# Performance work log

Measured on AMD Instinct MI355X. Metric: run time of the kernel, lower is better.

## Reference

```python
import jax, jax.numpy as jnp
import numpy as np

N = 50000       # nodes
E = 1600000     # edges (avg degree 32)
DIN = 64
DOUT = 64
DE = 16
ATT_SLOPE = 0.2   # leaky_relu slope inside attention (GAT standard)
ACT_SLOPE = 0.01  # F.leaky_relu default between layers


def setup_inputs() -> dict:
    key = jax.random.key(0)
    ks = jax.random.split(key, 16)

    def lin(k, i, o):
        return jax.random.normal(k, (i, o), jnp.float32) / np.sqrt(i).astype(np.float32)

    def vec(k, d):
        return jax.random.normal(k, (d,), jnp.float32) / np.sqrt(d).astype(np.float32)

    return {
        "X": jax.random.normal(ks[0], (N, DIN), jnp.float32),
        "edge_index": jax.random.randint(ks[1], (2, E), 0, N),
        "edge_attr": jax.random.normal(ks[2], (E, DE), jnp.float32),
        # layer 1 params
        "W1": lin(ks[3], DIN, DOUT), "We1": lin(ks[4], DE, DOUT),
        "as1": vec(ks[5], DOUT), "ad1": vec(ks[6], DOUT), "ae1": vec(ks[7], DOUT),
        "b1": jnp.zeros((DOUT,), jnp.float32),
        # layer 2 params
        "W2": lin(ks[8], DOUT, DOUT), "We2": lin(ks[9], DE, DOUT),
        "as2": vec(ks[10], DOUT), "ad2": vec(ks[11], DOUT), "ae2": vec(ks[12], DOUT),
        "b2": jnp.zeros((DOUT,), jnp.float32),
    }


def _gat_conv(x, src, dst, edge_attr, W, We, a_s, a_d, a_e, b):
    """GATConv with edge features, softmax attention over dst neighborhoods, max aggregation."""
    n = x.shape[0]
    h = x @ W                      # [N, DOUT]
    e = edge_attr @ We             # [E, DOUT]
    # per-edge attention logits
    logits = jax.nn.leaky_relu((h @ a_s)[src] + (h @ a_d)[dst] + e @ a_e, ATT_SLOPE)  # [E]
    # numerically-stable segment softmax over destination node
    m = jax.ops.segment_max(logits, dst, num_segments=n)      # [N]
    p = jnp.exp(logits - m[dst])                               # [E]
    s = jax.ops.segment_sum(p, dst, num_segments=n)            # [N]
    att = p / jnp.maximum(s[dst], 1e-16)                       # [E]
    msg = (h[src] + e) * att[:, None]                          # [E, DOUT]
    out = jax.ops.segment_max(msg, dst, num_segments=n)        # [N, DOUT], -inf for empty
    out = jnp.where(jnp.isfinite(out), out, 0.0)
    return out + b


def reference(X, edge_index, edge_attr,
              W1, We1, as1, ad1, ae1, b1,
              W2, We2, as2, ad2, ae2, b2):
    src, dst = edge_index[0], edge_index[1]
    c1 = _gat_conv(X, src, dst, edge_attr, W1, We1, as1, ad1, ae1, b1)
    c1 = jax.nn.leaky_relu(c1, ACT_SLOPE)
    c2 = _gat_conv(c1, src, dst, edge_attr, W2, We2, as2, ad2, ae2, b2)
    c2 = jax.nn.leaky_relu(c2, ACT_SLOPE)
    return c2
```

## Files before the change

### kernel.cpp

```cpp
#include <hip/hip_runtime.h>
#include <cstdint>
#include <cstddef>

#define NN 50000
#define EE 1600000
#define D  64
#define DE 16

typedef __attribute__((ext_vector_type(2))) float vf2;

__device__ __forceinline__ float bf2f(unsigned short u) {
    return __uint_as_float(((unsigned)u) << 16);
}
__device__ __forceinline__ unsigned short f2bf(float f) {
    unsigned u = __float_as_uint(f);
    unsigned r = u + 0x7FFFu + ((u >> 16) & 1u);
    return (unsigned short)(r >> 16);
}

#define HI_ILP 4
__global__ __launch_bounds__(256) void k_hist(const int* __restrict__ dst,
                                              int* __restrict__ counts) {
    int base = blockIdx.x * (256 * HI_ILP) + threadIdx.x;
    int dd[HI_ILP]; bool v[HI_ILP];
    #pragma unroll
    for (int j = 0; j < HI_ILP; j++) {
        int e = base + j * 256;
        v[j] = (e < EE);
        dd[j] = dst[v[j] ? e : 0];
    }
    #pragma unroll
    for (int j = 0; j < HI_ILP; j++)
        if (v[j]) atomicAdd(&counts[dd[j]], 1);
}

__global__ __launch_bounds__(256) void k_scanA(const int* counts, int* bsum) {
    __shared__ int tmp[256];
    int t = threadIdx.x, i = blockIdx.x * 256 + t;
    tmp[t] = (i < NN) ? counts[i] : 0;
    __syncthreads();
    for (int off = 128; off; off >>= 1) {
        if (t < off) tmp[t] += tmp[t + off];
        __syncthreads();
    }
    if (t == 0) bsum[blockIdx.x] = tmp[0];
}

__global__ __launch_bounds__(256) void k_scanB(int* bsum, int nchunks,
                                               const float* We1, const float* ae1,
                                               const float* We2, const float* ae2,
                                               float* wae) {
    __shared__ int tmp[256];
    int t = threadIdx.x;
    int v = (t < nchunks) ? bsum[t] : 0;
    tmp[t] = v; __syncthreads();
    for (int off = 1; off < 256; off <<= 1) {
        int x = (t >= off) ? tmp[t - off] : 0;
        __syncthreads();
        tmp[t] += x;
        __syncthreads();
    }
    if (t < nchunks) bsum[t] = tmp[t] - v;
    if (t < 32) {
        const float* We = (t < 16) ? We1 : We2;
        const float* ae = (t < 16) ? ae1 : ae2;
        int k = t & 15;
        float acc = 0.f;
        #pragma unroll
        for (int c = 0; c < 64; c++) acc += We[k * 64 + c] * ae[c];
        wae[t] = acc;
    }
}

__global__ __launch_bounds__(256) void k_scanC(const int* counts, const int* bsumex,
                                               int* offsets, int* cursor) {
    __shared__ int tmp[256];
    int t = threadIdx.x, i = blockIdx.x * 256 + t;
    int v = (i < NN) ? counts[i] : 0;
    tmp[t] = v; __syncthreads();
    for (int off = 1; off < 256; off <<= 1) {
        int x = (t >= off) ? tmp[t - off] : 0;
        __syncthreads();
        tmp[t] += x;
        __syncthreads();
    }
    int excl = tmp[t] - v + bsumex[blockIdx.x];
    if (i < NN) { offsets[i] = excl; cursor[i] = excl; }
}

#define SC_ILP 8
__global__ __launch_bounds__(256) void k_scatter(const int* __restrict__ src,
                                                 const int* __restrict__ dst,
                                                 int* __restrict__ cursor,
                                                 int2* __restrict__ recs) {
    int t = threadIdx.x;
    int base = blockIdx.x * (256 * SC_ILP) + t;
    int dd[SC_ILP], ss[SC_ILP], pos[SC_ILP];
    bool v[SC_ILP];
    #pragma unroll
    for (int j = 0; j < SC_ILP; j++) {
        int e = base + j * 256;
        v[j] = (e < EE);
        int ec = v[j] ? e : 0;
        dd[j] = dst[ec];
        ss[j] = src[ec];
    }
    #pragma unroll
    for (int j = 0; j < SC_ILP; j++)
        if (v[j]) pos[j] = atomicAdd(&cursor[dd[j]], 1);
    #pragma unroll
    for (int j = 0; j < SC_ILP; j++)
        if (v[j]) recs[pos[j]] = make_int2(ss[j], base + j * 256);
}

template<int IN_BF16>
__global__ __launch_bounds__(256, 4) void k_gemm(const void* xin, const float* W,
                                                 const float* a_s, const float* a_d,
                                                 unsigned short* h, float* hs, float* hd) {
    int t = threadIdx.x, lane = t & 63;
    int wid0 = blockIdx.x * 4 + (t >> 6);
    float Wcol[64];
    #pragma unroll
    for (int k = 0; k < 64; k++) Wcol[k] = W[k * 64 + lane];
    float asl = a_s[lane], adl = a_d[lane];
    for (int n0 = wid0; n0 < NN; n0 += 4096) {
        int n = __builtin_amdgcn_readfirstlane(n0);
        float acc = 0.f;
        if (IN_BF16) {
            const uint4* xr = (const uint4*)((const unsigned short*)xin + (size_t)n * 64);
            #pragma unroll
            for (int q = 0; q < 8; q++) {
                uint4 u = xr[q];
                unsigned uu[4] = {u.x, u.y, u.z, u.w};
                #pragma unroll
                for (int j = 0; j < 4; j++) {
                    acc += bf2f((unsigned short)(uu[j] & 0xFFFFu)) * Wcol[q * 8 + 2 * j];
                    acc += bf2f((unsigned short)(uu[j] >> 16))     * Wcol[q * 8 + 2 * j + 1];
                }
            }
        } else {
            const float4* xr = (const float4*)((const float*)xin + (size_t)n * 64);
            #pragma unroll
            for (int q = 0; q < 16; q++) {
                float4 u = xr[q];
                acc += u.x * Wcol[4 * q]     + u.y * Wcol[4 * q + 1]
                     + u.z * Wcol[4 * q + 2] + u.w * Wcol[4 * q + 3];
            }
        }
        h[(size_t)n * 64 + lane] = f2bf(acc);
        float ps = acc * asl, pd = acc * adl;
        #pragma unroll
        for (int off = 32; off; off >>= 1) {
            ps += __shfl_xor(ps, off);
            pd += __shfl_xor(pd, off);
        }
        if (lane == 0) { hs[n] = ps; hd[n] = pd; }
    }
}

template<int L2>
__global__ __launch_bounds__(256, 3) void k_gat(const int2* __restrict__ recs,
                                                const int* __restrict__ offsets,
                                                const int* __restrict__ counts,
                                                const float* __restrict__ hs,
                                                const float* __restrict__ hd,
                                                const unsigned short* __restrict__ h,
                                                const float* __restrict__ ea,
                                                const float* __restrict__ wae,
                                                const float* __restrict__ We,
                                                const float* __restrict__ b,
                                                void* __restrict__ outv) {
    __shared__ float4 eal[4][4][64];
    __shared__ float2 arx[4][64];
    int t = threadIdx.x, lane = t & 63, wv = t >> 6;
    int g = lane >> 4, cl = lane & 15;

    vf2 Wp[32];
    #pragma unroll
    for (int kp = 0; kp < 8; kp++) {
        float4 wa = *(const float4*)(We + (2 * kp) * 64 + 4 * cl);
        float4 wb = *(const float4*)(We + (2 * kp + 1) * 64 + 4 * cl);
        Wp[kp].x      = wa.x; Wp[kp].y      = wb.x;
        Wp[8 + kp].x  = wa.y; Wp[8 + kp].y  = wb.y;
        Wp[16 + kp].x = wa.z; Wp[16 + kp].y = wb.z;
        Wp[24 + kp].x = wa.w; Wp[24 + kp].y = wb.w;
    }
    float waer[16];
    {
        const float4* wp4 = (const float4*)(wae + L2 * 16);
        float4 w0 = wp4[0], w1 = wp4[1], w2 = wp4[2], w3 = wp4[3];
        waer[0]=w0.x; waer[1]=w0.y; waer[2]=w0.z; waer[3]=w0.w;
        waer[4]=w1.x; waer[5]=w1.y; waer[6]=w1.z; waer[7]=w1.w;
        waer[8]=w2.x; waer[9]=w2.y; waer[10]=w2.z; waer[11]=w2.w;
        waer[12]=w3.x; waer[13]=w3.y; waer[14]=w3.z; waer[15]=w3.w;
    }

    int d = blockIdx.x * 4 + wv;
    int start = offsets[d];
    int deg = counts[d];

    if (deg == 0) {
        if (g == 0) {
            float4 bl = *(const float4*)(b + 4 * cl);
            float o0 = (bl.x >= 0.f) ? bl.x : 0.01f * bl.x;
            float o1 = (bl.y >= 0.f) ? bl.y : 0.01f * bl.y;
            float o2 = (bl.z >= 0.f) ? bl.z : 0.01f * bl.z;
            float o3 = (bl.w >= 0.f) ? bl.w : 0.01f * bl.w;
            size_t oidx = (size_t)d * D + 4 * cl;
            if (L2) *(float4*)((float*)outv + oidx) = make_float4(o0, o1, o2, o3);
            else {
                ushort4 ov = {f2bf(o0), f2bf(o1), f2bf(o2), f2bf(o3)};
                *(ushort4*)((unsigned short*)outv + oidx) = ov;
            }
        }
        return;
    }

    float hdv = hd[d];
    bool fast = (deg <= 64);
    float m, invs;

    float ninf = -__builtin_inff();
    float a0 = ninf, a1 = ninf, a2 = ninf, a3 = ninf;

    if (fast) {
        float lg = ninf;
        if (lane < deg) {
            int2 r = recs[start + lane];
            const float4* ep = (const float4*)(ea + (size_t)r.y * DE);
            float4 q0 = ep[0], q1 = ep[1], q2 = ep[2], q3 = ep[3];
            float hsv = hs[r.x];
            eal[wv][0][lane] = q0; eal[wv][1][lane] = q1;
            eal[wv][2][lane] = q2; eal[wv][3][lane] = q3;
            arx[wv][lane].y = __int_as_float(r.x);
            float ev[16] = {q0.x, q0.y, q0.z, q0.w, q1.x, q1.y, q1.z, q1.w,
                            q2.x, q2.y, q2.z, q2.w, q3.x, q3.y, q3.z, q3.w};
            float ee = 0.f;
            #pragma unroll
            for (int j = 0; j < 16; j++) ee += ev[j] * waer[j];
            lg = hsv + hdv + ee;
            lg = (lg >= 0.f) ? lg : 0.2f * lg;
        }

        bool vC = (g < deg);
        int jC = vC ? g : 0;
        int rxC = __float_as_int(arx[wv][jC].y);
        ushort4 hvC = *(const ushort4*)(h + (size_t)rxC * D + 4 * cl);

        m = lg;
        #pragma unroll
        for (int off = 32; off; off >>= 1) m = fmaxf(m, __shfl_xor(m, off));
        float p = __expf(lg - m);
        float s = p;
        #pragma unroll
        for (int off = 32; off; off >>= 1) s += __shfl_xor(s, off);
        invs = 1.0f / fmaxf(s, 1e-16f);
        if (lane < deg) arx[wv][lane].x = p * invs;

        float attC = arx[wv][jC].x;

        for (int i = 0; i < deg; i += 4) {
            int jn = i + 4 + g;
            bool vN = (jn < deg);
            int jN = vN ? jn : 0;
            float2 arN = arx[wv][jN];
            int rxN = __float_as_int(arN.y);
            ushort4 hvN = *(const ushort4*)(h + (size_t)rxN * D + 4 * cl);

            vf2 acA = {0.f, 0.f}, acB = {0.f, 0.f}, acC2 = {0.f, 0.f}, acD = {0.f, 0.f};
            #pragma unroll
            for (int kq = 0; kq < 4; kq++) {
                float4 q = eal[wv][kq][jC];
                vf2 eA; eA.x = q.x; eA.y = q.y;
                vf2 eB; eB.x = q.z; eB.y = q.w;
                acA += eA * Wp[2 * kq];       acA += eB * Wp[2 * kq + 1];
                acB += eA * Wp[8 + 2 * kq];   acB += eB * Wp[8 + 2 * kq + 1];
                acC2 += eA * Wp[16 + 2 * kq]; acC2 += eB * Wp[16 + 2 * kq + 1];
                acD += eA * Wp[24 + 2 * kq];  acD += eB * Wp[24 + 2 * kq + 1];
            }
            float e0 = acA.x + acA.y, e1 = acB.x + acB.y;
            float e2 = acC2.x + acC2.y, e3 = acD.x + acD.y;
            float o0 = (bf2f(hvC.x) + e0) * attC;
            float o1 = (bf2f(hvC.y) + e1) * attC;
            float o2 = (bf2f(hvC.z) + e2) * attC;
            float o3 = (bf2f(hvC.w) + e3) * attC;
            if (vC) {
                a0 = fmaxf(a0, o0); a1 = fmaxf(a1, o1);
                a2 = fmaxf(a2, o2); a3 = fmaxf(a3, o3);
            }
            attC = arN.x; hvC = hvN; vC = vN; jC = jN;
        }
    } else {
        float mm = ninf, s = 0.f;
        for (int i = lane; i < deg; i += 64) {
            int2 r = recs[start + i];
            const float4* ep = (const float4*)(ea + (size_t)r.y * DE);
            float4 q0 = ep[0], q1 = ep[1], q2 = ep[2], q3 = ep[3];
            float ev[16] = {q0.x, q0.y, q0.z, q0.w, q1.x, q1.y, q1.z, q1.w,
                            q2.x, q2.y, q2.z, q2.w, q3.x, q3.y, q3.z, q3.w};
            float ee = 0.f;
            #pragma unroll
            for (int j = 0; j < 16; j++) ee += ev[j] * waer[j];
            float lg = hs[r.x] + hdv + ee;
            lg = (lg >= 0.f) ? lg : 0.2f * lg;
            float mn = fmaxf(mm, lg);
            s = ((mm == mn) ? s : s * __expf(mm - mn)) + __expf(lg - mn);
            mm = mn;
        }
        #pragma unroll
        for (int off = 32; off; off >>= 1) {
            float m2 = __shfl_xor(mm, off);
            float s2 = __shfl_xor(s, off);
            float mn = fmaxf(mm, m2);
            float sa = (mm == mn) ? s : s * __expf(mm - mn);
            float sb = (m2 == mn) ? s2 : s2 * __expf(m2 - mn);
            s = sa + sb;
            mm = mn;
        }
        m = mm;
        invs = 1.0f / fmaxf(s, 1e-16f);

        for (int i = 0; i < deg; i += 4) {
            int j = i + g;
            bool valid = (j < deg);
            int jc = valid ? j : 0;
            int2 r = recs[start + jc];
            const float4* ep = (const float4*)(ea + (size_t)r.y * DE);
            float4 q0 = ep[0], q1 = ep[1], q2 = ep[2], q3 = ep[3];
            float ev[16] = {q0.x, q0.y, q0.z, q0.w, q1.x, q1.y, q1.z, q1.w,
                            q2.x, q2.y, q2.z, q2.w, q3.x, q3.y, q3.z, q3.w};
            float ee = 0.f;
            #pragma unroll
            for (int j2 = 0; j2 < 16; j2++) ee += ev[j2] * waer[j2];
            float lg = hs[r.x] + hdv + ee;
            lg = (lg >= 0.f) ? lg : 0.2f * lg;
            float att = __expf(lg - m) * invs;
            ushort4 hv = *(const ushort4*)(h + (size_t)r.x * D + 4 * cl);
            float4 qs[4] = {q0, q1, q2, q3};
            vf2 acA = {0.f, 0.f}, acB = {0.f, 0.f}, acC2 = {0.f, 0.f}, acD = {0.f, 0.f};
            #pragma unroll
            for (int kq = 0; kq < 4; kq++) {
                float4 q = qs[kq];
                vf2 eA; eA.x = q.x; eA.y = q.y;
                vf2 eB; eB.x = q.z; eB.y = q.w;
                acA += eA * Wp[2 * kq];       acA += eB * Wp[2 * kq + 1];
                acB += eA * Wp[8 + 2 * kq];   acB += eB * Wp[8 + 2 * kq + 1];
                acC2 += eA * Wp[16 + 2 * kq]; acC2 += eB * Wp[16 + 2 * kq + 1];
                acD += eA * Wp[24 + 2 * kq];  acD += eB * Wp[24 + 2 * kq + 1];
            }
            float e0 = acA.x + acA.y, e1 = acB.x + acB.y;
            float e2 = acC2.x + acC2.y, e3 = acD.x + acD.y;
            float o0 = (bf2f(hv.x) + e0) * att;
            float o1 = (bf2f(hv.y) + e1) * att;
            float o2 = (bf2f(hv.z) + e2) * att;
            float o3 = (bf2f(hv.w) + e3) * att;
            if (valid) {
                a0 = fmaxf(a0, o0); a1 = fmaxf(a1, o1);
                a2 = fmaxf(a2, o2); a3 = fmaxf(a3, o3);
            }
        }
    }

    #pragma unroll
    for (int off = 16; off <= 32; off <<= 1) {
        a0 = fmaxf(a0, __shfl_xor(a0, off));
        a1 = fmaxf(a1, __shfl_xor(a1, off));
        a2 = fmaxf(a2, __shfl_xor(a2, off));
        a3 = fmaxf(a3, __shfl_xor(a3, off));
    }

    if (g == 0) {
        float4 bl = *(const float4*)(b + 4 * cl);
        float o0 = a0 + bl.x, o1 = a1 + bl.y;
        float o2 = a2 + bl.z, o3 = a3 + bl.w;
        o0 = (o0 >= 0.f) ? o0 : 0.01f * o0;
        o1 = (o1 >= 0.f) ? o1 : 0.01f * o1;
        o2 = (o2 >= 0.f) ? o2 : 0.01f * o2;
        o3 = (o3 >= 0.f) ? o3 : 0.01f * o3;
        size_t oidx = (size_t)d * D + 4 * cl;
        if (L2) {
            *(float4*)((float*)outv + oidx) = make_float4(o0, o1, o2, o3);
        } else {
            ushort4 ov = {f2bf(o0), f2bf(o1), f2bf(o2), f2bf(o3)};
            *(ushort4*)((unsigned short*)outv + oidx) = ov;
        }
    }
}

extern "C" void kernel_launch(void* const* d_in, const int* in_sizes, int n_in,
                              void* d_out, int out_size, void* d_ws, size_t ws_size,
                              hipStream_t stream) {
    const float* X   = (const float*)d_in[0];
    const int*   eix = (const int*)d_in[1];
    const float* ea  = (const float*)d_in[2];
    const float* W1  = (const float*)d_in[3];
    const float* We1 = (const float*)d_in[4];
    const float* as1 = (const float*)d_in[5];
    const float* ad1 = (const float*)d_in[6];
    const float* ae1 = (const float*)d_in[7];
    const float* b1  = (const float*)d_in[8];
    const float* W2  = (const float*)d_in[9];
    const float* We2 = (const float*)d_in[10];
    const float* as2 = (const float*)d_in[11];
    const float* ad2 = (const float*)d_in[12];
    const float* ae2 = (const float*)d_in[13];
    const float* b2  = (const float*)d_in[14];

    const int* src = eix;
    const int* dst = eix + EE;

    char* w = (char*)d_ws;
    int2* recs = (int2*)w;               w += (size_t)EE * 8;
    unsigned short* hA = (unsigned short*)w; w += (size_t)NN * D * 2;
    unsigned short* hB = (unsigned short*)w; w += (size_t)NN * D * 2;
    float* hs = (float*)w;               w += (size_t)NN * 4;
    float* hd = (float*)w;               w += (size_t)NN * 4;
    int* counts = (int*)w;               w += (size_t)NN * 4;
    int* offsets = (int*)w;              w += (size_t)NN * 4;
    int* cursor = (int*)w;               w += (size_t)NN * 4;
    int* bsum = (int*)w;                 w += 256 * 4;
    float* wae = (float*)w;              w += 32 * 4;

    const int nchunks = (NN + 255) / 256;
    const int nhblk = (EE + 256 * HI_ILP - 1) / (256 * HI_ILP);
    const int nsblk = (EE + 256 * SC_ILP - 1) / (256 * SC_ILP);

    hipMemsetAsync(counts, 0, (size_t)NN * 4, stream);
    k_hist<<<nhblk, 256, 0, stream>>>(dst, counts);
    k_scanA<<<nchunks, 256, 0, stream>>>(counts, bsum);
    k_scanB<<<1, 256, 0, stream>>>(bsum, nchunks, We1, ae1, We2, ae2, wae);
    k_scanC<<<nchunks, 256, 0, stream>>>(counts, bsum, offsets, cursor);
    k_scatter<<<nsblk, 256, 0, stream>>>(src, dst, cursor, recs);

    k_gemm<0><<<1024, 256, 0, stream>>>(X, W1, as1, ad1, hA, hs, hd);
    k_gat<0><<<NN / 4, 256, 0, stream>>>(recs, offsets, counts, hs, hd, hA, ea,
                                         wae, We1, b1, hB);
    k_gemm<1><<<1024, 256, 0, stream>>>(hB, W2, as2, ad2, hB, hs, hd);
    k_gat<1><<<NN / 4, 256, 0, stream>>>(recs, offsets, counts, hs, hd, hB, ea,
                                         wae, We2, b2, (float*)d_out);
}
```

Baseline: 614.7 us.

## Precompute per-edge attention terms in scatter and deepen gather prefetch

The scatter kernel now computes the edge-feature attention term for both layers and stores it in a widened 16-byte CSR record, together with the source index and edge id. The GAT kernels read this precomputed term instead of re-reading the 16-float edge attributes and doing a dot product in the logit pass. In the fast path, the h-row gather is software-pipelined two iterations ahead instead of one. The trade is doubled record storage and bandwidth and an extra edge_attr read in scatter, against less edge_attr traffic and arithmetic in both GAT layers.

```diff
diff --git a/kernel.cpp b/kernel.cpp
--- a/kernel.cpp
+++ b/kernel.cpp
@@ -46,10 +46,7 @@
     if (t == 0) bsum[blockIdx.x] = tmp[0];
 }
 
-__global__ __launch_bounds__(256) void k_scanB(int* bsum, int nchunks,
-                                               const float* We1, const float* ae1,
-                                               const float* We2, const float* ae2,
-                                               float* wae) {
+__global__ __launch_bounds__(256) void k_scanB(int* bsum, int nchunks) {
     __shared__ int tmp[256];
     int t = threadIdx.x;
     int v = (t < nchunks) ? bsum[t] : 0;
@@ -61,15 +58,6 @@
         __syncthreads();
     }
     if (t < nchunks) bsum[t] = tmp[t] - v;
-    if (t < 32) {
-        const float* We = (t < 16) ? We1 : We2;
-        const float* ae = (t < 16) ? ae1 : ae2;
-        int k = t & 15;
-        float acc = 0.f;
-        #pragma unroll
-        for (int c = 0; c < 64; c++) acc += We[k * 64 + c] * ae[c];
-        wae[t] = acc;
-    }
 }
 
 __global__ __launch_bounds__(256) void k_scanC(const int* counts, const int* bsumex,
@@ -91,9 +79,29 @@
 #define SC_ILP 8
 __global__ __launch_bounds__(256) void k_scatter(const int* __restrict__ src,
                                                  const int* __restrict__ dst,
+                                                 const float* __restrict__ ea,
+                                                 const float* __restrict__ We1,
+                                                 const float* __restrict__ ae1,
+                                                 const float* __restrict__ We2,
+                                                 const float* __restrict__ ae2,
                                                  int* __restrict__ cursor,
-                                                 int2* __restrict__ recs) {
+                                                 int4* __restrict__ recs) {
+    __shared__ float wsh[32];
     int t = threadIdx.x;
+    if (t < 32) {
+        const float* We = (t < 16) ? We1 : We2;
+        const float* ae = (t < 16) ? ae1 : ae2;
+        int k = t & 15;
+        float acc = 0.f;
+        #pragma unroll
+        for (int c = 0; c < 64; c++) acc += We[k * 64 + c] * ae[c];
+        wsh[t] = acc;
+    }
+    __syncthreads();
+    float w1r[16], w2r[16];
+    #pragma unroll
+    for (int j = 0; j < 16; j++) { w1r[j] = wsh[j]; w2r[j] = wsh[16 + j]; }
+
     int base = blockIdx.x * (256 * SC_ILP) + t;
     int dd[SC_ILP], ss[SC_ILP], pos[SC_ILP];
     bool v[SC_ILP];
@@ -109,8 +117,21 @@
     for (int j = 0; j < SC_ILP; j++)
         if (v[j]) pos[j] = atomicAdd(&cursor[dd[j]], 1);
     #pragma unroll
-    for (int j = 0; j < SC_ILP; j++)
-        if (v[j]) recs[pos[j]] = make_int2(ss[j], base + j * 256);
+    for (int j = 0; j < SC_ILP; j++) {
+        if (!v[j]) continue;
+        int e = base + j * 256;
+        const float4* rp = (const float4*)(ea + (size_t)e * DE);
+        float4 q0 = rp[0], q1 = rp[1], q2 = rp[2], q3 = rp[3];
+        float ev[16] = {q0.x, q0.y, q0.z, q0.w, q1.x, q1.y, q1.z, q1.w,
+                        q2.x, q2.y, q2.z, q2.w, q3.x, q3.y, q3.z, q3.w};
+        float e1 = 0.f, e2 = 0.f;
+        #pragma unroll
+        for (int k2 = 0; k2 < 16; k2++) {
+            e1 += ev[k2] * w1r[k2];
+            e2 += ev[k2] * w2r[k2];
+        }
+        recs[pos[j]] = make_int4(ss[j], e, __float_as_int(e1), __float_as_int(e2));
+    }
 }
 
 template<int IN_BF16>
@@ -159,14 +180,13 @@
 }
 
 template<int L2>
-__global__ __launch_bounds__(256, 3) void k_gat(const int2* __restrict__ recs,
+__global__ __launch_bounds__(256, 3) void k_gat(const int4* __restrict__ recs,
                                                 const int* __restrict__ offsets,
                                                 const int* __restrict__ counts,
                                                 const float* __restrict__ hs,
                                                 const float* __restrict__ hd,
                                                 const unsigned short* __restrict__ h,
                                                 const float* __restrict__ ea,
-                                                const float* __restrict__ wae,
                                                 const float* __restrict__ We,
                                                 const float* __restrict__ b,
                                                 void* __restrict__ outv) {
@@ -184,15 +204,6 @@
         Wp[8 + kp].x  = wa.y; Wp[8 + kp].y  = wb.y;
         Wp[16 + kp].x = wa.z; Wp[16 + kp].y = wb.z;
         Wp[24 + kp].x = wa.w; Wp[24 + kp].y = wb.w;
-    }
-    float waer[16];
-    {
-        const float4* wp4 = (const float4*)(wae + L2 * 16);
-        float4 w0 = wp4[0], w1 = wp4[1], w2 = wp4[2], w3 = wp4[3];
-        waer[0]=w0.x; waer[1]=w0.y; waer[2]=w0.z; waer[3]=w0.w;
-        waer[4]=w1.x; waer[5]=w1.y; waer[6]=w1.z; waer[7]=w1.w;
-        waer[8]=w2.x; waer[9]=w2.y; waer[10]=w2.z; waer[11]=w2.w;
-        waer[12]=w3.x; waer[13]=w3.y; waer[14]=w3.z; waer[15]=w3.w;
     }
 
     int d = blockIdx.x * 4 + wv;
@@ -226,26 +237,26 @@
     if (fast) {
         float lg = ninf;
         if (lane < deg) {
-            int2 r = recs[start + lane];
+            int4 r = recs[start + lane];
             const float4* ep = (const float4*)(ea + (size_t)r.y * DE);
             float4 q0 = ep[0], q1 = ep[1], q2 = ep[2], q3 = ep[3];
             float hsv = hs[r.x];
             eal[wv][0][lane] = q0; eal[wv][1][lane] = q1;
             eal[wv][2][lane] = q2; eal[wv][3][lane] = q3;
             arx[wv][lane].y = __int_as_float(r.x);
-            float ev[16] = {q0.x, q0.y, q0.z, q0.w, q1.x, q1.y, q1.z, q1.w,
-                            q2.x, q2.y, q2.z, q2.w, q3.x, q3.y, q3.z, q3.w};
-            float ee = 0.f;
-            #pragma unroll
-            for (int j = 0; j < 16; j++) ee += ev[j] * waer[j];
+            float ee = __int_as_float(L2 ? r.w : r.z);
             lg = hsv + hdv + ee;
             lg = (lg >= 0.f) ? lg : 0.2f * lg;
         }
 
         bool vC = (g < deg);
         int jC = vC ? g : 0;
+        bool vN = (4 + g < deg);
+        int jN = vN ? 4 + g : 0;
         int rxC = __float_as_int(arx[wv][jC].y);
+        int rxN = __float_as_int(arx[wv][jN].y);
         ushort4 hvC = *(const ushort4*)(h + (size_t)rxC * D + 4 * cl);
+        ushort4 hvN = *(const ushort4*)(h + (size_t)rxN * D + 4 * cl);
 
         m = lg;
         #pragma unroll
@@ -258,14 +269,15 @@
         if (lane < deg) arx[wv][lane].x = p * invs;
 
         float attC = arx[wv][jC].x;
+        float attN = arx[wv][jN].x;
 
         for (int i = 0; i < deg; i += 4) {
-            int jn = i + 4 + g;
-            bool vN = (jn < deg);
-            int jN = vN ? jn : 0;
-            float2 arN = arx[wv][jN];
-            int rxN = __float_as_int(arN.y);
-            ushort4 hvN = *(const ushort4*)(h + (size_t)rxN * D + 4 * cl);
+            int jnn = i + 8 + g;
+            bool vNN = (jnn < deg);
+            int jNN = vNN ? jnn : 0;
+            float2 arNN = arx[wv][jNN];
+            int rxNN = __float_as_int(arNN.y);
+            ushort4 hvNN = *(const ushort4*)(h + (size_t)rxNN * D + 4 * cl);
 
             vf2 acA = {0.f, 0.f}, acB = {0.f, 0.f}, acC2 = {0.f, 0.f}, acD = {0.f, 0.f};
             #pragma unroll
@@ -288,19 +300,14 @@
                 a0 = fmaxf(a0, o0); a1 = fmaxf(a1, o1);
                 a2 = fmaxf(a2, o2); a3 = fmaxf(a3, o3);
             }
-            attC = arN.x; hvC = hvN; vC = vN; jC = jN;
+            jC = jN; vC = vN; hvC = hvN; attC = attN;
+            jN = jNN; vN = vNN; hvN = hvNN; attN = arNN.x;
         }
     } else {
         float mm = ninf, s = 0.f;
         for (int i = lane; i < deg; i += 64) {
-            int2 r = recs[start + i];
-            const float4* ep = (const float4*)(ea + (size_t)r.y * DE);
-            float4 q0 = ep[0], q1 = ep[1], q2 = ep[2], q3 = ep[3];
-            float ev[16] = {q0.x, q0.y, q0.z, q0.w, q1.x, q1.y, q1.z, q1.w,
-                            q2.x, q2.y, q2.z, q2.w, q3.x, q3.y, q3.z, q3.w};
-            float ee = 0.f;
-            #pragma unroll
-            for (int j = 0; j < 16; j++) ee += ev[j] * waer[j];
+            int4 r = recs[start + i];
+            float ee = __int_as_float(L2 ? r.w : r.z);
             float lg = hs[r.x] + hdv + ee;
             lg = (lg >= 0.f) ? lg : 0.2f * lg;
             float mn = fmaxf(mm, lg);
@@ -324,17 +331,13 @@
             int j = i + g;
             bool valid = (j < deg);
             int jc = valid ? j : 0;
-            int2 r = recs[start + jc];
-            const float4* ep = (const float4*)(ea + (size_t)r.y * DE);
-            float4 q0 = ep[0], q1 = ep[1], q2 = ep[2], q3 = ep[3];
-            float ev[16] = {q0.x, q0.y, q0.z, q0.w, q1.x, q1.y, q1.z, q1.w,
-                            q2.x, q2.y, q2.z, q2.w, q3.x, q3.y, q3.z, q3.w};
-            float ee = 0.f;
-            #pragma unroll
-            for (int j2 = 0; j2 < 16; j2++) ee += ev[j2] * waer[j2];
+            int4 r = recs[start + jc];
+            float ee = __int_as_float(L2 ? r.w : r.z);
             float lg = hs[r.x] + hdv + ee;
             lg = (lg >= 0.f) ? lg : 0.2f * lg;
             float att = __expf(lg - m) * invs;
+            const float4* ep = (const float4*)(ea + (size_t)r.y * DE);
+            float4 q0 = ep[0], q1 = ep[1], q2 = ep[2], q3 = ep[3];
             ushort4 hv = *(const ushort4*)(h + (size_t)r.x * D + 4 * cl);
             float4 qs[4] = {q0, q1, q2, q3};
             vf2 acA = {0.f, 0.f}, acB = {0.f, 0.f}, acC2 = {0.f, 0.f}, acD = {0.f, 0.f};
@@ -410,7 +413,7 @@
     const int* dst = eix + EE;
 
     char* w = (char*)d_ws;
-    int2* recs = (int2*)w;               w += (size_t)EE * 8;
+    int4* recs = (int4*)w;               w += (size_t)EE * 16;
     unsigned short* hA = (unsigned short*)w; w += (size_t)NN * D * 2;
     unsigned short* hB = (unsigned short*)w; w += (size_t)NN * D * 2;
     float* hs = (float*)w;               w += (size_t)NN * 4;
@@ -419,7 +422,6 @@
     int* offsets = (int*)w;              w += (size_t)NN * 4;
     int* cursor = (int*)w;               w += (size_t)NN * 4;
     int* bsum = (int*)w;                 w += 256 * 4;
-    float* wae = (float*)w;              w += 32 * 4;
 
     const int nchunks = (NN + 255) / 256;
     const int nhblk = (EE + 256 * HI_ILP - 1) / (256 * HI_ILP);
@@ -428,14 +430,13 @@
     hipMemsetAsync(counts, 0, (size_t)NN * 4, stream);
     k_hist<<<nhblk, 256, 0, stream>>>(dst, counts);
     k_scanA<<<nchunks, 256, 0, stream>>>(counts, bsum);
-    k_scanB<<<1, 256, 0, stream>>>(bsum, nchunks, We1, ae1, We2, ae2, wae);
+    k_scanB<<<1, 256, 0, stream>>>(bsum, nchunks);
     k_scanC<<<nchunks, 256, 0, stream>>>(counts, bsum, offsets, cursor);
-    k_scatter<<<nsblk, 256, 0, stream>>>(src, dst, cursor, recs);
+    k_scatter<<<nsblk, 256, 0, stream>>>(src, dst, ea, We1, ae1, We2, ae2, cursor, recs);
 
     k_gemm<0><<<1024, 256, 0, stream>>>(X, W1, as1, ad1, hA, hs, hd);
-    k_gat<0><<<NN / 4, 256, 0, stream>>>(recs, offsets, counts, hs, hd, hA, ea,
-                                         wae, We1, b1, hB);
+    k_gat<0><<<NN / 4, 256, 0, stream>>>(recs, offsets, counts, hs, hd, hA, ea, We1, b1, hB);
     k_gemm<1><<<1024, 256, 0, stream>>>(hB, W2, as2, ad2, hB, hs, hd);
-    k_gat<1><<<NN / 4, 256, 0, stream>>>(recs, offsets, counts, hs, hd, hB, ea,
-                                         wae, We2, b2, (float*)d_out);
-}
+    k_gat<1><<<NN / 4, 256, 0, stream>>>(recs, offsets, counts, hs, hd, hB, ea, We2, b2,
+                                         (float*)d_out);
+}
```

New measurement: 627.2 us. 1.02x slower.
